# Kernel optimization log

Hardware: AMD Instinct MI355X
Metric: run time of the kernel (lower is better)

Reference implementation:

```python
import jax, jax.numpy as jnp
import numpy as np
import math

B, T, D_MODEL, N_HEADS, K_CONV = 2, 2048, 2048, 16, 4
HEAD_DIM = D_MODEL // N_HEADS
EPS_GN = 1e-5


def setup_inputs() -> dict:
    key = jax.random.key(0)
    ks = jax.random.split(key, 16)
    s = 0.02
    # gamma bias init per reset_parameters (decays 0.9..0.9999 per head)
    min_d, max_d = 0.9, 0.9999
    tgt = 1.0 - np.exp(np.linspace(math.log(1 - min_d), math.log(1 - max_d), N_HEADS))
    gamma_bias = np.log(tgt / (1 - tgt)).astype(np.float32)
    return {
        "x": jax.random.normal(ks[0], (B, T, D_MODEL), jnp.float32),
        "Wq": jax.random.normal(ks[1], (D_MODEL, D_MODEL), jnp.float32) * s,
        "Wk": jax.random.normal(ks[2], (D_MODEL, D_MODEL), jnp.float32) * s,
        "Wv": jax.random.normal(ks[3], (D_MODEL, D_MODEL), jnp.float32) * s,
        "Wo": jax.random.normal(ks[4], (D_MODEL, D_MODEL), jnp.float32) * s,
        "conv_w": jax.random.normal(ks[5], (D_MODEL, K_CONV), jnp.float32) * 0.1,
        "conv_b": jnp.zeros((D_MODEL,), jnp.float32),
        "Wig": jax.random.normal(ks[6], (D_MODEL, D_MODEL), jnp.float32) * s,
        "b_ig": jnp.zeros((D_MODEL,), jnp.float32),
        "Wog": jax.random.normal(ks[7], (D_MODEL, D_MODEL), jnp.float32) * s,
        "b_og": jnp.zeros((D_MODEL,), jnp.float32),
        "Wg": jnp.zeros((N_HEADS, D_MODEL), jnp.float32),
        "b_g": jnp.asarray(gamma_bias),
        "gn_w": jnp.ones((D_MODEL,), jnp.float32),
        "gn_b": jnp.zeros((D_MODEL,), jnp.float32),
        "mn_w": jnp.ones((D_MODEL,), jnp.float32),
        "mn_b": jnp.zeros((D_MODEL,), jnp.float32),
    }


def _group_norm(x2d, w, b, groups, eps):
    # x2d: [N, C], normalize per group of C//groups channels
    N, C = x2d.shape
    xg = x2d.reshape(N, groups, C // groups)
    mu = xg.mean(-1, keepdims=True)
    var = ((xg - mu) ** 2).mean(-1, keepdims=True)
    xn = ((xg - mu) * jax.lax.rsqrt(var + eps)).reshape(N, C)
    return xn * w + b


def _causal_depthwise_conv(x, w, b):
    # x: [B,T,C], w: [C,K], b: [C] -> [B,T,C] causal depthwise conv + silu
    xt = jnp.transpose(x, (0, 2, 1))  # [B,C,T]
    xp = jnp.pad(xt, ((0, 0), (0, 0), (K_CONV - 1, 0)))
    y = jax.lax.conv_general_dilated(
        xp, w[:, None, :], (1,), "VALID",
        feature_group_count=D_MODEL,
        dimension_numbers=("NCH", "OIH", "NCH"))
    y = y + b[None, :, None]
    return jax.nn.silu(jnp.transpose(y, (0, 2, 1)))


def _l2norm(t):
    n = jnp.sqrt(jnp.sum(t * t, axis=-1, keepdims=True))
    return t / jnp.maximum(n, 1e-12)


def reference(x, Wq, Wk, Wv, Wo, conv_w, conv_b, Wig, b_ig, Wog, b_og, Wg, b_g, gn_w, gn_b, mn_w, mn_b):
    Bq, Tq, C = x.shape
    x_conv = _causal_depthwise_conv(x, conv_w, conv_b)  # [B,T,C]

    q = _l2norm((x @ Wq.T).reshape(Bq, Tq, N_HEADS, HEAD_DIM))
    k = _l2norm((x @ Wk.T).reshape(Bq, Tq, N_HEADS, HEAD_DIM))
    v = (x @ Wv.T).reshape(Bq, Tq, N_HEADS, HEAD_DIM)

    input_gate = jax.nn.sigmoid(x_conv @ Wig.T + b_ig).reshape(Bq, Tq, N_HEADS, HEAD_DIM)
    gamma = jax.nn.sigmoid(x_conv @ Wg.T + b_g).reshape(Bq, Tq, N_HEADS, 1)

    # gated elementwise linear recurrence: h_t = gamma_t * h_{t-1} + i_t * (k_t * v_t)
    bterm = input_gate * k * v                       # [B,T,H,D]
    aterm = jnp.broadcast_to(gamma, bterm.shape)     # [B,T,H,D]

    def scan_op(c1, c2):
        a1, b1 = c1
        a2, b2 = c2
        return (a1 * a2, a2 * b1 + b2)

    _, mem = jax.lax.associative_scan(scan_op, (aterm, bterm), axis=1)
    next_rnn_state = mem[:, -1]

    mem_n = _group_norm(mem.reshape(Bq * Tq, D_MODEL), mn_w, mn_b, N_HEADS, EPS_GN)
    mem_n = mem_n.reshape(Bq, Tq, N_HEADS, HEAD_DIM)

    out = (mem_n * q).reshape(Bq * Tq, C)
    out = _group_norm(out, gn_w, gn_b, N_HEADS, EPS_GN).reshape(Bq, Tq, C)

    output_gate = jax.nn.sigmoid(x_conv @ Wog.T + b_og)
    out = (out * output_gate) @ Wo.T

    new_conv_cache = jnp.transpose(x, (0, 2, 1))[:, :, -(K_CONV - 1):]
    return out, next_rnn_state, new_conv_cache
```

## Files before the change

kernel.cpp:

```cpp
#include <hip/hip_runtime.h>
#include <math.h>

#define B_ 2
#define T_ 2048
#define D_ 2048
#define H_ 16
#define M_ 4096
#define TD_ (T_ * D_)
#define EPS_ 1e-5f
#define NC_ 32
#define CL_ 64

typedef __bf16 bf16x8 __attribute__((ext_vector_type(8)));
typedef float f32x4 __attribute__((ext_vector_type(4)));

__device__ __forceinline__ float sigm(float z) { return 1.f / (1.f + __expf(-z)); }

__device__ __forceinline__ ushort f2bf(float f) {
    union { float f; uint u; } x; x.f = f;
    uint r = x.u + 0x7fffu + ((x.u >> 16) & 1u);
    return (ushort)(r >> 16);
}
__device__ __forceinline__ float bflo(uint u) { union { uint u; float f; } x; x.u = u << 16; return x.f; }
__device__ __forceinline__ float bfhi(uint u) { union { uint u; float f; } x; x.u = u & 0xffff0000u; return x.f; }

__device__ __forceinline__ void gload_lds16(const void* g, void* l) {
    __builtin_amdgcn_global_load_lds((const __attribute__((address_space(1))) void*)g,
                                     (__attribute__((address_space(3))) void*)l, 16, 0, 0);
}

template <int IMM>
__device__ __forceinline__ bf16x8 dsr(uint addr) {
    int4 d;
    asm volatile("ds_read_b128 %0, %1 offset:%2" : "=v"(d) : "v"(addr), "n"(IMM));
    return __builtin_bit_cast(bf16x8, d);
}
#define LGKM0 do { asm volatile("s_waitcnt lgkmcnt(0)" ::: "memory"); __builtin_amdgcn_sched_barrier(0); } while (0)
#define SBAR  __builtin_amdgcn_s_barrier()

__global__ __launch_bounds__(256) void cvtw_kernel(
    const float* __restrict__ Wq, const float* __restrict__ Wk, const float* __restrict__ Wv,
    const float* __restrict__ Wig, const float* __restrict__ Wog, const float* __restrict__ Wo,
    ushort* __restrict__ W6)
{
    const int z = blockIdx.y;
    const float* src = z == 0 ? Wq : z == 1 ? Wk : z == 2 ? Wv : z == 3 ? Wig : z == 4 ? Wog : Wo;
    const int i4 = (blockIdx.x * 256 + threadIdx.x) * 4;
    float4 f = *(const float4*)(src + i4);
    ushort4 o; o.x = f2bf(f.x); o.y = f2bf(f.y); o.z = f2bf(f.z); o.w = f2bf(f.w);
    *(ushort4*)(W6 + (size_t)z * ((size_t)D_ * D_) + i4) = o;
}

__global__ __launch_bounds__(256) void conv_kernel(
    const float* __restrict__ x, const float* __restrict__ cw, const float* __restrict__ cb,
    ushort* __restrict__ xb, ushort* __restrict__ xcb)
{
    const int idx = blockIdx.x * 256 + threadIdx.x;
    const int c = idx & (D_ - 1);
    const int t = (idx >> 11) & (T_ - 1);
    const float* w = cw + c * 4;
    const float x3 = x[idx];
    float a = cb[c] + w[3] * x3;
    if (t >= 1) a += w[2] * x[idx - D_];
    if (t >= 2) a += w[1] * x[idx - 2 * D_];
    if (t >= 3) a += w[0] * x[idx - 3 * D_];
    xb[idx] = f2bf(x3);
    xcb[idx] = f2bf(a * sigm(a));
}

template <bool BF16OUT>
__device__ __forceinline__ void gemm256_body(
    const ushort* __restrict__ A, const ushort* __restrict__ Bw,
    ushort* __restrict__ Cb, float* __restrict__ Cf, int bx, int by)
{
    extern __shared__ char smem[];
    const int tid = threadIdx.x;
    const int lane = tid & 63, wid = tid >> 6;
    const int wm = wid >> 2, wn = wid & 3;
    const int l15 = lane & 15, l4 = lane >> 4;
    const int brow = by * 256, bcol = bx * 256;

    const int srow = tid >> 3;
    const int scol = ((tid & 7) * 8) ^ (((tid >> 3) & 7) << 3);
    const uint sldso = (uint)tid * 16;

    f32x4 acc[8][4] = {};

    #pragma unroll
    for (int tt = 0; tt < 2; ++tt) {
        const uint bo = (uint)tt * 65536u;
        const int k0 = tt * 64;
        #pragma unroll
        for (int j = 0; j < 4; ++j)
            gload_lds16(A + (size_t)(brow + j * 64 + srow) * D_ + (k0 + scol),
                        smem + bo + j * 8192 + sldso);
        #pragma unroll
        for (int j = 0; j < 4; ++j)
            gload_lds16(Bw + (size_t)(bcol + j * 64 + srow) * D_ + (k0 + scol),
                        smem + bo + 32768u + j * 8192 + sldso);
    }
    asm volatile("s_waitcnt vmcnt(8)" ::: "memory");
    SBAR;

    const uint r7  = (uint)((l15 & 7) << 4);
    const uint ca0 = (uint)(l4 * 16) ^ r7;
    const uint ca1 = (uint)(64 + l4 * 16) ^ r7;
    const uint arow = (uint)(wm * 128 + l15) * 128u;
    const uint brw  = 32768u + (uint)(wn * 64 + l15) * 128u;
    const uint ldsbase = (uint)(size_t)smem;

    #pragma unroll 2
    for (int t = 0; t < 32; ++t) {
        const uint bo = ldsbase + (uint)(t & 1) * 65536u;
        const uint ab0 = bo + arow + ca0, ab1 = bo + arow + ca1;
        const uint bb0 = bo + brw + ca0,  bb1 = bo + brw + ca1;
        bf16x8 a0[8], a1[8], b0[4], b1[4];
        a0[0] = dsr<0>(ab0);        a0[1] = dsr<0>(ab1);
        a0[2] = dsr<2048>(ab0);     a0[3] = dsr<2048>(ab1);
        a0[4] = dsr<4096>(ab0);     a0[5] = dsr<4096>(ab1);
        a0[6] = dsr<6144>(ab0);     a0[7] = dsr<6144>(ab1);
        b0[0] = dsr<0>(bb0);        b0[1] = dsr<0>(bb1);
        b0[2] = dsr<2048>(bb0);     b0[3] = dsr<2048>(bb1);
        SBAR;
        LGKM0;
        __builtin_amdgcn_s_setprio(1);
        #pragma unroll
        for (int ks = 0; ks < 2; ++ks)
            #pragma unroll
            for (int m = 0; m < 4; ++m)
                #pragma unroll
                for (int n = 0; n < 2; ++n)
                    acc[m][n] = __builtin_amdgcn_mfma_f32_16x16x32_bf16(
                        a0[m * 2 + ks], b0[n * 2 + ks], acc[m][n], 0, 0, 0);
        __builtin_amdgcn_sched_barrier(0);
        __builtin_amdgcn_s_setprio(0);
        SBAR;
        b1[0] = dsr<4096>(bb0);     b1[1] = dsr<4096>(bb1);
        b1[2] = dsr<6144>(bb0);     b1[3] = dsr<6144>(bb1);
        SBAR;
        LGKM0;
        __builtin_amdgcn_s_setprio(1);
        #pragma unroll
        for (int ks = 0; ks < 2; ++ks)
            #pragma unroll
            for (int m = 0; m < 4; ++m)
                #pragma unroll
                for (int n = 0; n < 2; ++n)
                    acc[m][2 + n] = __builtin_amdgcn_mfma_f32_16x16x32_bf16(
                        a0[m * 2 + ks], b1[n * 2 + ks], acc[m][2 + n], 0, 0, 0);
        __builtin_amdgcn_sched_barrier(0);
        __builtin_amdgcn_s_setprio(0);
        SBAR;
        a1[0] = dsr<8192>(ab0);      a1[1] = dsr<8192>(ab1);
        a1[2] = dsr<10240>(ab0);     a1[3] = dsr<10240>(ab1);
        a1[4] = dsr<12288>(ab0);     a1[5] = dsr<12288>(ab1);
        a1[6] = dsr<14336>(ab0);     a1[7] = dsr<14336>(ab1);
        SBAR;
        LGKM0;
        __builtin_amdgcn_s_setprio(1);
        #pragma unroll
        for (int ks = 0; ks < 2; ++ks)
            #pragma unroll
            for (int m = 0; m < 4; ++m)
                #pragma unroll
                for (int n = 0; n < 2; ++n)
                    acc[4 + m][n] = __builtin_amdgcn_mfma_f32_16x16x32_bf16(
                        a1[m * 2 + ks], b0[n * 2 + ks], acc[4 + m][n], 0, 0, 0);
        __builtin_amdgcn_sched_barrier(0);
        __builtin_amdgcn_s_setprio(0);
        SBAR;
        if (t + 2 < 32) {
            const uint bo2 = (uint)(t & 1) * 65536u;
            const int k0 = (t + 2) * 64;
            #pragma unroll
            for (int j = 0; j < 4; ++j)
                gload_lds16(A + (size_t)(brow + j * 64 + srow) * D_ + (k0 + scol),
                            smem + bo2 + j * 8192 + sldso);
            #pragma unroll
            for (int j = 0; j < 4; ++j)
                gload_lds16(Bw + (size_t)(bcol + j * 64 + srow) * D_ + (k0 + scol),
                            smem + bo2 + 32768u + j * 8192 + sldso);
        }
        SBAR;
        __builtin_amdgcn_s_setprio(1);
        #pragma unroll
        for (int ks = 0; ks < 2; ++ks)
            #pragma unroll
            for (int m = 0; m < 4; ++m)
                #pragma unroll
                for (int n = 0; n < 2; ++n)
                    acc[4 + m][2 + n] = __builtin_amdgcn_mfma_f32_16x16x32_bf16(
                        a1[m * 2 + ks], b1[n * 2 + ks], acc[4 + m][2 + n], 0, 0, 0);
        __builtin_amdgcn_sched_barrier(0);
        __builtin_amdgcn_s_setprio(0);
        if (t < 31) {
            if (t < 30) asm volatile("s_waitcnt vmcnt(8)" ::: "memory");
            else        asm volatile("s_waitcnt vmcnt(0)" ::: "memory");
            SBAR;
        }
    }

    #pragma unroll
    for (int m = 0; m < 8; ++m)
        #pragma unroll
        for (int n = 0; n < 4; ++n) {
            const int row = brow + wm * 128 + m * 16 + l4 * 4;
            const int col = bcol + wn * 64 + n * 16 + l15;
            #pragma unroll
            for (int r = 0; r < 4; ++r) {
                if (BF16OUT) Cb[(size_t)(row + r) * D_ + col] = f2bf(acc[m][n][r]);
                else         Cf[(size_t)(row + r) * D_ + col] = acc[m][n][r];
            }
        }
}

__global__ __launch_bounds__(512, 2) void gemm5_kernel(
    const ushort* __restrict__ xb, const ushort* __restrict__ xcb,
    const ushort* __restrict__ W6, ushort* __restrict__ Obuf)
{
    const int g = (blockIdx.z * 16 + blockIdx.y) * 8 + blockIdx.x;
    const int ns = (g & 7) * 80 + (g >> 3);
    const int z = ns >> 7, rem = ns & 127, by = rem >> 3, bx = rem & 7;
    const ushort* Aop = (z < 3) ? xb : xcb;
    gemm256_body<true>(Aop, W6 + (size_t)z * ((size_t)D_ * D_),
                       Obuf + (size_t)z * ((size_t)M_ * D_), nullptr, bx, by);
}

__global__ __launch_bounds__(512, 2) void gemm_out_kernel(
    const ushort* __restrict__ gated, const ushort* __restrict__ W6, float* __restrict__ out)
{
    const int g = blockIdx.y * 8 + blockIdx.x;
    const int ns = (g & 7) * 16 + (g >> 3);
    const int by = ns >> 3, bx = ns & 7;
    gemm256_body<false>(gated, W6 + (size_t)5 * ((size_t)D_ * D_), nullptr, out, bx, by);
}

__global__ __launch_bounds__(256) void gamma_kernel(
    const ushort* __restrict__ xcb, const float* __restrict__ Wg,
    const float* __restrict__ bg, float* __restrict__ gamma)
{
    __shared__ ushort xs[8 * D_];
    const int tid = threadIdx.x;
    const int tok0 = blockIdx.x * 8;
    const uint4* gsrc = (const uint4*)(xcb + (size_t)tok0 * D_);
    #pragma unroll
    for (int j = 0; j < 8; ++j)
        ((uint4*)xs)[j * 256 + tid] = gsrc[j * 256 + tid];
    __syncthreads();
    const int tok = tid >> 5;
    const int h = (tid >> 1) & 15;
    const int half = tid & 1;
    const ushort* xr = xs + tok * D_ + half * 1024;
    const float* wr = Wg + (size_t)h * D_ + half * 1024;
    float acc = 0.f;
    #pragma unroll 4
    for (int i = 0; i < 1024; i += 8) {
        uint4 u = *(const uint4*)(xr + i);
        float4 w0 = *(const float4*)(wr + i);
        float4 w1 = *(const float4*)(wr + i + 4);
        acc += bflo(u.x) * w0.x + bfhi(u.x) * w0.y + bflo(u.y) * w0.z + bfhi(u.y) * w0.w;
        acc += bflo(u.z) * w1.x + bfhi(u.z) * w1.y + bflo(u.w) * w1.z + bfhi(u.w) * w1.w;
    }
    acc += __shfl_xor(acc, 1);
    if (!half) gamma[(size_t)(tok0 + tok) * H_ + h] = sigm(acc + bg[h]);
}

__global__ __launch_bounds__(256) void bterm_kernel(
    const ushort* __restrict__ kb, const ushort* __restrict__ vb,
    const ushort* __restrict__ igb, const float* __restrict__ big,
    float* __restrict__ bt)
{
    const int token = blockIdx.x;
    const int tid = threadIdx.x;
    const int c0 = tid * 8;
    const size_t base = (size_t)token * D_ + c0;
    uint4 ku = *(const uint4*)(kb + base);
    uint4 vu = *(const uint4*)(vb + base);
    uint4 iu = *(const uint4*)(igb + base);
    float kf[8] = { bflo(ku.x), bfhi(ku.x), bflo(ku.y), bfhi(ku.y),
                    bflo(ku.z), bfhi(ku.z), bflo(ku.w), bfhi(ku.w) };
    float vf[8] = { bflo(vu.x), bfhi(vu.x), bflo(vu.y), bfhi(vu.y),
                    bflo(vu.z), bfhi(vu.z), bflo(vu.w), bfhi(vu.w) };
    float gf[8] = { bflo(iu.x), bfhi(iu.x), bflo(iu.y), bfhi(iu.y),
                    bflo(iu.z), bfhi(iu.z), bflo(iu.w), bfhi(iu.w) };
    float ss = 0.f;
    #pragma unroll
    for (int j = 0; j < 8; ++j) ss += kf[j] * kf[j];
    #pragma unroll
    for (int o = 1; o < 16; o <<= 1) ss += __shfl_xor(ss, o);
    const float sc = 1.f / fmaxf(sqrtf(ss), 1e-12f);
    float ot[8];
    #pragma unroll
    for (int j = 0; j < 8; ++j)
        ot[j] = sigm(gf[j] + big[c0 + j]) * (kf[j] * sc) * vf[j];
    float4 o0 = { ot[0], ot[1], ot[2], ot[3] };
    float4 o1 = { ot[4], ot[5], ot[6], ot[7] };
    *(float4*)(bt + base) = o0;
    *(float4*)(bt + base + 4) = o1;
}

__global__ __launch_bounds__(256) void scan1_kernel(
    const float* __restrict__ bt, const float* __restrict__ gam,
    float* __restrict__ Ab, float* __restrict__ Sb)
{
    const int c = blockIdx.x * 256 + threadIdx.x;
    const int ch = blockIdx.y, b = blockIdx.z;
    const int h = c >> 7;
    const float* g = gam + ((size_t)b * T_ + ch * CL_) * H_ + h;
    const float* p = bt + ((size_t)b * T_ + ch * CL_) * D_ + c;
    float a = 1.f, s = 0.f;
    #pragma unroll 8
    for (int i = 0; i < CL_; ++i) {
        const float gv = g[(size_t)i * H_];
        s = fmaf(gv, s, p[(size_t)i * D_]);
        a *= gv;
    }
    const size_t o = ((size_t)b * NC_ + ch) * D_ + c;
    Ab[o] = a; Sb[o] = s;
}

__global__ __launch_bounds__(256) void scan2_kernel(
    const float* __restrict__ Ab, const float* __restrict__ Sb, float* __restrict__ carry)
{
    const int idx = blockIdx.x * 256 + threadIdx.x;
    const int b = idx >> 11, c = idx & (D_ - 1);
    float run = 0.f;
    #pragma unroll
    for (int ch = 0; ch < NC_; ++ch) {
        const size_t o = ((size_t)b * NC_ + ch) * D_ + c;
        carry[o] = run;
        run = fmaf(Ab[o], run, Sb[o]);
    }
}

__global__ __launch_bounds__(256) void scan3_kernel(
    float* __restrict__ bt, const float* __restrict__ gam, const float* __restrict__ carry)
{
    const int c = blockIdx.x * 256 + threadIdx.x;
    const int ch = blockIdx.y, b = blockIdx.z;
    const int h = c >> 7;
    const float* g = gam + ((size_t)b * T_ + ch * CL_) * H_ + h;
    float* p = bt + ((size_t)b * T_ + ch * CL_) * D_ + c;
    float m = carry[((size_t)b * NC_ + ch) * D_ + c];
    #pragma unroll 8
    for (int i = 0; i < CL_; ++i) {
        m = fmaf(g[(size_t)i * H_], m, p[(size_t)i * D_]);
        p[(size_t)i * D_] = m;
    }
}

__global__ __launch_bounds__(256) void norm_kernel(
    const float* __restrict__ mem, const ushort* __restrict__ qb,
    const ushort* __restrict__ ogb, const float* __restrict__ bog,
    const float* __restrict__ mnw, const float* __restrict__ mnb,
    const float* __restrict__ gnw, const float* __restrict__ gnb,
    ushort* __restrict__ gated, float* __restrict__ rnn)
{
    const int token = blockIdx.x;
    const int tid = threadIdx.x;
    const int c0 = tid * 8;
    const size_t base = (size_t)token * D_ + c0;
    float mm[8];
    { float4 a = *(const float4*)(mem + base); float4 b2 = *(const float4*)(mem + base + 4);
      mm[0]=a.x; mm[1]=a.y; mm[2]=a.z; mm[3]=a.w; mm[4]=b2.x; mm[5]=b2.y; mm[6]=b2.z; mm[7]=b2.w; }
    float s1 = 0.f, s2 = 0.f;
    #pragma unroll
    for (int j = 0; j < 8; ++j) { s1 += mm[j]; s2 += mm[j] * mm[j]; }
    #pragma unroll
    for (int o = 1; o < 16; o <<= 1) { s1 += __shfl_xor(s1, o); s2 += __shfl_xor(s2, o); }
    const float mu = s1 * (1.f / 128.f);
    const float inv = 1.f / sqrtf(fmaxf(s2 * (1.f / 128.f) - mu * mu, 0.f) + EPS_);
    uint4 qu = *(const uint4*)(qb + base);
    float qf[8] = { bflo(qu.x), bfhi(qu.x), bflo(qu.y), bfhi(qu.y),
                    bflo(qu.z), bfhi(qu.z), bflo(qu.w), bfhi(qu.w) };
    float qs = 0.f;
    #pragma unroll
    for (int j = 0; j < 8; ++j) qs += qf[j] * qf[j];
    #pragma unroll
    for (int o = 1; o < 16; o <<= 1) qs += __shfl_xor(qs, o);
    const float qsc = 1.f / fmaxf(sqrtf(qs), 1e-12f);
    float ov[8]; float t1 = 0.f, t2 = 0.f;
    #pragma unroll
    for (int j = 0; j < 8; ++j) {
        const float mn = (mm[j] - mu) * inv * mnw[c0 + j] + mnb[c0 + j];
        ov[j] = mn * (qf[j] * qsc);
        t1 += ov[j]; t2 += ov[j] * ov[j];
    }
    #pragma unroll
    for (int o = 1; o < 16; o <<= 1) { t1 += __shfl_xor(t1, o); t2 += __shfl_xor(t2, o); }
    const float mu2 = t1 * (1.f / 128.f);
    const float inv2 = 1.f / sqrtf(fmaxf(t2 * (1.f / 128.f) - mu2 * mu2, 0.f) + EPS_);
    uint4 ou = *(const uint4*)(ogb + base);
    float of[8] = { bflo(ou.x), bfhi(ou.x), bflo(ou.y), bfhi(ou.y),
                    bflo(ou.z), bfhi(ou.z), bflo(ou.w), bfhi(ou.w) };
    uint pk[4];
    #pragma unroll
    for (int j2 = 0; j2 < 4; ++j2) {
        const int e0 = 2 * j2, e1 = 2 * j2 + 1;
        float g0 = ((ov[e0] - mu2) * inv2 * gnw[c0 + e0] + gnb[c0 + e0]) * sigm(of[e0] + bog[c0 + e0]);
        float g1 = ((ov[e1] - mu2) * inv2 * gnw[c0 + e1] + gnb[c0 + e1]) * sigm(of[e1] + bog[c0 + e1]);
        pk[j2] = (uint)f2bf(g0) | ((uint)f2bf(g1) << 16);
    }
    uint4 st = { pk[0], pk[1], pk[2], pk[3] };
    *(uint4*)(gated + base) = st;
    if ((token & (T_ - 1)) == T_ - 1) {
        float* r = rnn + (size_t)(token >> 11) * D_ + c0;
        float4 r0 = { mm[0], mm[1], mm[2], mm[3] };
        float4 r1 = { mm[4], mm[5], mm[6], mm[7] };
        *(float4*)r = r0; *(float4*)(r + 4) = r1;
    }
}

__global__ __launch_bounds__(256) void cache_kernel(const float* __restrict__ x, float* __restrict__ out)
{
    const int idx = blockIdx.x * 256 + threadIdx.x;
    if (idx >= B_ * D_ * 3) return;
    const int b = idx / (D_ * 3);
    const int rem = idx - b * (D_ * 3);
    const int c = rem / 3;
    const int j = rem - c * 3;
    out[idx] = x[((size_t)b * T_ + (T_ - 3 + j)) * D_ + c];
}

extern "C" void kernel_launch(void* const* d_in, const int* in_sizes, int n_in,
                              void* d_out, int out_size, void* d_ws, size_t ws_size,
                              hipStream_t stream)
{
    const float* x   = (const float*)d_in[0];
    const float* Wq  = (const float*)d_in[1];
    const float* Wk  = (const float*)d_in[2];
    const float* Wv  = (const float*)d_in[3];
    const float* Wo  = (const float*)d_in[4];
    const float* cw  = (const float*)d_in[5];
    const float* cb  = (const float*)d_in[6];
    const float* Wig = (const float*)d_in[7];
    const float* big = (const float*)d_in[8];
    const float* Wog = (const float*)d_in[9];
    const float* bog = (const float*)d_in[10];
    const float* Wg  = (const float*)d_in[11];
    const float* bg  = (const float*)d_in[12];
    const float* gnw = (const float*)d_in[13];
    const float* gnb = (const float*)d_in[14];
    const float* mnw = (const float*)d_in[15];
    const float* mnb = (const float*)d_in[16];

    char* ws = (char*)d_ws;
    ushort* W6   = (ushort*)ws;
    ushort* xb   = (ushort*)(ws + 50331648);
    ushort* xcb  = (ushort*)(ws + 50331648 + 16777216);
    ushort* Obuf = (ushort*)(ws + 50331648 + 2 * 16777216);
    float*  gam  = (float*)(ws + 50331648 + 7 * 16777216);
    float*  bt   = (float*)(ws + 50331648 + 7 * 16777216 + 262144);

    ushort* q    = Obuf;
    ushort* k    = Obuf + (size_t)M_ * D_;
    ushort* v    = Obuf + 2 * (size_t)M_ * D_;
    ushort* igp  = Obuf + 3 * (size_t)M_ * D_;
    ushort* ogp  = Obuf + 4 * (size_t)M_ * D_;
    ushort* gated = k;
    float*  Ab   = (float*)v;
    float*  Sb   = Ab + (size_t)B_ * NC_ * D_;
    float*  carry= Sb + (size_t)B_ * NC_ * D_;

    float* out  = (float*)d_out;
    float* rnn  = out + (size_t)M_ * D_;
    float* cach = rnn + B_ * D_;

    (void)hipFuncSetAttribute((const void*)gemm5_kernel,
                              hipFuncAttributeMaxDynamicSharedMemorySize, 131072);
    (void)hipFuncSetAttribute((const void*)gemm_out_kernel,
                              hipFuncAttributeMaxDynamicSharedMemorySize, 131072);

    cvtw_kernel<<<dim3(4096, 6), 256, 0, stream>>>(Wq, Wk, Wv, Wig, Wog, Wo, W6);
    conv_kernel<<<dim3(M_ * D_ / 256), 256, 0, stream>>>(x, cw, cb, xb, xcb);
    gemm5_kernel<<<dim3(8, 16, 5), 512, 131072, stream>>>(xb, xcb, W6, Obuf);
    gamma_kernel<<<dim3(M_ / 8), 256, 0, stream>>>(xcb, Wg, bg, gam);
    bterm_kernel<<<dim3(M_), 256, 0, stream>>>(k, v, igp, big, bt);
    scan1_kernel<<<dim3(8, NC_, 2), 256, 0, stream>>>(bt, gam, Ab, Sb);
    scan2_kernel<<<dim3(16), 256, 0, stream>>>(Ab, Sb, carry);
    scan3_kernel<<<dim3(8, NC_, 2), 256, 0, stream>>>(bt, gam, carry);
    norm_kernel<<<dim3(M_), 256, 0, stream>>>(bt, q, ogp, bog, mnw, mnb, gnw, gnb, gated, rnn);
    gemm_out_kernel<<<dim3(8, 16), 512, 131072, stream>>>(gated, W6, out);
    cache_kernel<<<dim3(48), 256, 0, stream>>>(x, cach);
}
```

Measured before the change: 433.6 us.

## Shrink GEMM block tile to 256x128 to double block count

Changes the bf16 MFMA GEMM tile from 256x256 to 256x128. Each wave now owns a 64x64 sub-tile instead of 128x64, and the A-second-half load and MFMA phases are removed. LDS drops to 96KB per block and the grids double, with block-swizzle mapping adjusted to match. This aims to improve CU occupancy and wave balance for the 5-way projection and output GEMMs. In exchange it lowers arithmetic intensity and reloads A tiles more often.

```diff
diff --git a/kernel.cpp b/kernel.cpp
--- a/kernel.cpp
+++ b/kernel.cpp
@@ -76,45 +76,46 @@
     extern __shared__ char smem[];
     const int tid = threadIdx.x;
     const int lane = tid & 63, wid = tid >> 6;
-    const int wm = wid >> 2, wn = wid & 3;
+    const int wm = wid >> 1, wn = wid & 1;
     const int l15 = lane & 15, l4 = lane >> 4;
-    const int brow = by * 256, bcol = bx * 256;
+    const int brow = by * 256, bcol = bx * 128;
 
     const int srow = tid >> 3;
     const int scol = ((tid & 7) * 8) ^ (((tid >> 3) & 7) << 3);
     const uint sldso = (uint)tid * 16;
 
-    f32x4 acc[8][4] = {};
-
-    #pragma unroll
-    for (int tt = 0; tt < 2; ++tt) {
-        const uint bo = (uint)tt * 65536u;
-        const int k0 = tt * 64;
-        #pragma unroll
-        for (int j = 0; j < 4; ++j)
-            gload_lds16(A + (size_t)(brow + j * 64 + srow) * D_ + (k0 + scol),
-                        smem + bo + j * 8192 + sldso);
-        #pragma unroll
-        for (int j = 0; j < 4; ++j)
-            gload_lds16(Bw + (size_t)(bcol + j * 64 + srow) * D_ + (k0 + scol),
-                        smem + bo + 32768u + j * 8192 + sldso);
-    }
-    asm volatile("s_waitcnt vmcnt(8)" ::: "memory");
+    f32x4 acc[4][4] = {};
+
+    #define STAGE6(bufo, k0)                                                         \
+        do {                                                                         \
+            _Pragma("unroll")                                                        \
+            for (int j = 0; j < 4; ++j)                                              \
+                gload_lds16(A + (size_t)(brow + j * 64 + srow) * D_ + ((k0) + scol), \
+                            smem + (bufo) + j * 8192 + sldso);                       \
+            _Pragma("unroll")                                                        \
+            for (int j = 0; j < 2; ++j)                                              \
+                gload_lds16(Bw + (size_t)(bcol + j * 64 + srow) * D_ + ((k0) + scol),\
+                            smem + (bufo) + 32768u + j * 8192 + sldso);              \
+        } while (0)
+
+    STAGE6(0u, 0);
+    STAGE6(49152u, 64);
+    asm volatile("s_waitcnt vmcnt(6)" ::: "memory");
     SBAR;
 
     const uint r7  = (uint)((l15 & 7) << 4);
     const uint ca0 = (uint)(l4 * 16) ^ r7;
     const uint ca1 = (uint)(64 + l4 * 16) ^ r7;
-    const uint arow = (uint)(wm * 128 + l15) * 128u;
+    const uint arow = (uint)(wm * 64 + l15) * 128u;
     const uint brw  = 32768u + (uint)(wn * 64 + l15) * 128u;
     const uint ldsbase = (uint)(size_t)smem;
 
     #pragma unroll 2
     for (int t = 0; t < 32; ++t) {
-        const uint bo = ldsbase + (uint)(t & 1) * 65536u;
+        const uint bo = ldsbase + (uint)(t & 1) * 49152u;
         const uint ab0 = bo + arow + ca0, ab1 = bo + arow + ca1;
         const uint bb0 = bo + brw + ca0,  bb1 = bo + brw + ca1;
-        bf16x8 a0[8], a1[8], b0[4], b1[4];
+        bf16x8 a0[8], b0[4], b1[4];
         a0[0] = dsr<0>(ab0);        a0[1] = dsr<0>(ab1);
         a0[2] = dsr<2048>(ab0);     a0[3] = dsr<2048>(ab1);
         a0[4] = dsr<4096>(ab0);     a0[5] = dsr<4096>(ab1);
@@ -150,61 +151,23 @@
                         a0[m * 2 + ks], b1[n * 2 + ks], acc[m][2 + n], 0, 0, 0);
         __builtin_amdgcn_sched_barrier(0);
         __builtin_amdgcn_s_setprio(0);
-        SBAR;
-        a1[0] = dsr<8192>(ab0);      a1[1] = dsr<8192>(ab1);
-        a1[2] = dsr<10240>(ab0);     a1[3] = dsr<10240>(ab1);
-        a1[4] = dsr<12288>(ab0);     a1[5] = dsr<12288>(ab1);
-        a1[6] = dsr<14336>(ab0);     a1[7] = dsr<14336>(ab1);
-        SBAR;
-        LGKM0;
-        __builtin_amdgcn_s_setprio(1);
-        #pragma unroll
-        for (int ks = 0; ks < 2; ++ks)
-            #pragma unroll
-            for (int m = 0; m < 4; ++m)
-                #pragma unroll
-                for (int n = 0; n < 2; ++n)
-                    acc[4 + m][n] = __builtin_amdgcn_mfma_f32_16x16x32_bf16(
-                        a1[m * 2 + ks], b0[n * 2 + ks], acc[4 + m][n], 0, 0, 0);
-        __builtin_amdgcn_sched_barrier(0);
-        __builtin_amdgcn_s_setprio(0);
-        SBAR;
-        if (t + 2 < 32) {
-            const uint bo2 = (uint)(t & 1) * 65536u;
-            const int k0 = (t + 2) * 64;
-            #pragma unroll
-            for (int j = 0; j < 4; ++j)
-                gload_lds16(A + (size_t)(brow + j * 64 + srow) * D_ + (k0 + scol),
-                            smem + bo2 + j * 8192 + sldso);
-            #pragma unroll
-            for (int j = 0; j < 4; ++j)
-                gload_lds16(Bw + (size_t)(bcol + j * 64 + srow) * D_ + (k0 + scol),
-                            smem + bo2 + 32768u + j * 8192 + sldso);
+        if (t <= 29) {
+            const uint bo2 = (uint)(t & 1) * 49152u;
+            STAGE6(bo2, (t + 2) * 64);
         }
-        SBAR;
-        __builtin_amdgcn_s_setprio(1);
-        #pragma unroll
-        for (int ks = 0; ks < 2; ++ks)
-            #pragma unroll
-            for (int m = 0; m < 4; ++m)
-                #pragma unroll
-                for (int n = 0; n < 2; ++n)
-                    acc[4 + m][2 + n] = __builtin_amdgcn_mfma_f32_16x16x32_bf16(
-                        a1[m * 2 + ks], b1[n * 2 + ks], acc[4 + m][2 + n], 0, 0, 0);
-        __builtin_amdgcn_sched_barrier(0);
-        __builtin_amdgcn_s_setprio(0);
         if (t < 31) {
-            if (t < 30) asm volatile("s_waitcnt vmcnt(8)" ::: "memory");
+            if (t < 30) asm volatile("s_waitcnt vmcnt(6)" ::: "memory");
             else        asm volatile("s_waitcnt vmcnt(0)" ::: "memory");
             SBAR;
         }
     }
-
-    #pragma unroll
-    for (int m = 0; m < 8; ++m)
+    #undef STAGE6
+
+    #pragma unroll
+    for (int m = 0; m < 4; ++m)
         #pragma unroll
         for (int n = 0; n < 4; ++n) {
-            const int row = brow + wm * 128 + m * 16 + l4 * 4;
+            const int row = brow + wm * 64 + m * 16 + l4 * 4;
             const int col = bcol + wn * 64 + n * 16 + l15;
             #pragma unroll
             for (int r = 0; r < 4; ++r) {
@@ -218,9 +181,9 @@
     const ushort* __restrict__ xb, const ushort* __restrict__ xcb,
     const ushort* __restrict__ W6, ushort* __restrict__ Obuf)
 {
-    const int g = (blockIdx.z * 16 + blockIdx.y) * 8 + blockIdx.x;
-    const int ns = (g & 7) * 80 + (g >> 3);
-    const int z = ns >> 7, rem = ns & 127, by = rem >> 3, bx = rem & 7;
+    const int g = (blockIdx.z * 16 + blockIdx.y) * 16 + blockIdx.x;
+    const int ns = (g & 7) * 160 + (g >> 3);
+    const int z = ns >> 8, rem = ns & 255, by = rem >> 4, bx = rem & 15;
     const ushort* Aop = (z < 3) ? xb : xcb;
     gemm256_body<true>(Aop, W6 + (size_t)z * ((size_t)D_ * D_),
                        Obuf + (size_t)z * ((size_t)M_ * D_), nullptr, bx, by);
@@ -229,9 +192,9 @@
 __global__ __launch_bounds__(512, 2) void gemm_out_kernel(
     const ushort* __restrict__ gated, const ushort* __restrict__ W6, float* __restrict__ out)
 {
-    const int g = blockIdx.y * 8 + blockIdx.x;
-    const int ns = (g & 7) * 16 + (g >> 3);
-    const int by = ns >> 3, bx = ns & 7;
+    const int g = blockIdx.y * 16 + blockIdx.x;
+    const int ns = (g & 7) * 32 + (g >> 3);
+    const int by = ns >> 4, bx = ns & 15;
     gemm256_body<false>(gated, W6 + (size_t)5 * ((size_t)D_ * D_), nullptr, out, bx, by);
 }
 
@@ -467,19 +430,19 @@
     float* cach = rnn + B_ * D_;
 
     (void)hipFuncSetAttribute((const void*)gemm5_kernel,
-                              hipFuncAttributeMaxDynamicSharedMemorySize, 131072);
+                              hipFuncAttributeMaxDynamicSharedMemorySize, 98304);
     (void)hipFuncSetAttribute((const void*)gemm_out_kernel,
-                              hipFuncAttributeMaxDynamicSharedMemorySize, 131072);
+                              hipFuncAttributeMaxDynamicSharedMemorySize, 98304);
 
     cvtw_kernel<<<dim3(4096, 6), 256, 0, stream>>>(Wq, Wk, Wv, Wig, Wog, Wo, W6);
     conv_kernel<<<dim3(M_ * D_ / 256), 256, 0, stream>>>(x, cw, cb, xb, xcb);
-    gemm5_kernel<<<dim3(8, 16, 5), 512, 131072, stream>>>(xb, xcb, W6, Obuf);
+    gemm5_kernel<<<dim3(16, 16, 5), 512, 98304, stream>>>(xb, xcb, W6, Obuf);
     gamma_kernel<<<dim3(M_ / 8), 256, 0, stream>>>(xcb, Wg, bg, gam);
     bterm_kernel<<<dim3(M_), 256, 0, stream>>>(k, v, igp, big, bt);
     scan1_kernel<<<dim3(8, NC_, 2), 256, 0, stream>>>(bt, gam, Ab, Sb);
     scan2_kernel<<<dim3(16), 256, 0, stream>>>(Ab, Sb, carry);
     scan3_kernel<<<dim3(8, NC_, 2), 256, 0, stream>>>(bt, gam, carry);
     norm_kernel<<<dim3(M_), 256, 0, stream>>>(bt, q, ogp, bog, mnw, mnb, gnw, gnb, gated, rnn);
-    gemm_out_kernel<<<dim3(8, 16), 512, 131072, stream>>>(gated, W6, out);
+    gemm_out_kernel<<<dim3(16, 16), 512, 98304, stream>>>(gated, W6, out);
     cache_kernel<<<dim3(48), 256, 0, stream>>>(x, cach);
 }
```

After: 394.6 us. 1.1x faster.
